# Performance work log

Measured on AMD Instinct MI355X. Metric: run time of the kernel, lower is better.

## Reference

```python
import jax, jax.numpy as jnp
import numpy as np

B, N, D = 512, 22, 3
H, TD, AD, L = 128, 32, 32, 4
SIGMA_DATA = 0.168
NORM_CONST = 1.0
E_IN = 2 * H + 1 + 2  # [h_i, h_j, radial, dist_sq, bond_mask]
NUM_ATOM_TYPES = 4
BONDS = [(0, 1), (1, 2), (1, 3), (1, 4), (4, 5), (4, 6), (6, 7), (6, 8), (8, 9), (8, 10),
         (10, 11), (10, 12), (10, 13), (8, 14), (14, 15), (14, 16), (16, 17), (16, 18),
         (18, 19), (18, 20), (18, 21)]
ATOM_TYPES = [0, 1, 0, 0, 1, 2, 3, 0, 1, 0, 1, 0, 0, 0, 1, 2, 3, 0, 1, 0, 0, 0]


def setup_inputs() -> dict:
    key = jax.random.key(0)
    ks = jax.random.split(key, 16)
    xt = jax.random.normal(ks[0], (B, N, D), jnp.float32)
    xt = xt - xt.mean(axis=1, keepdims=True)  # zero center of mass, per assert_mean_zero
    # EDM-style noise levels, strictly positive (log-normal as in compute_loss)
    t = jnp.exp(jax.random.normal(ks[1], (B,), jnp.float32) * 1.2 - 1.2)
    # fully connected edges without self-loops, batched with node offset b*N
    ii, jj = np.meshgrid(np.arange(N), np.arange(N), indexing='ij')
    msk = ii != jj
    ri, ci = ii[msk], jj[msk]  # (N*(N-1),)
    off = (np.arange(B) * N)[:, None]
    row = jnp.asarray((ri[None] + off).reshape(-1), jnp.int32)
    col = jnp.asarray((ci[None] + off).reshape(-1), jnp.int32)
    adj = np.zeros((N, N), np.float32)
    for a, b in BONDS:
        adj[a, b] = 1.0
        adj[b, a] = 1.0
    bond_mask = jnp.asarray(np.tile(adj[ri, ci], B)[:, None], jnp.float32)  # (E,1)
    atom_types = jnp.asarray(ATOM_TYPES, jnp.int32)

    def lin(k, fi, fo):
        return jax.random.normal(k, (fi, fo), jnp.float32) / np.sqrt(fi)

    def per_layer(k, fi, fo):
        return jax.random.normal(k, (L, fi, fo), jnp.float32) / np.sqrt(fi)

    z = lambda *s: jnp.zeros(s, jnp.float32)
    return dict(
        xt=xt, t=t,
        atom_table=jax.random.normal(ks[2], (NUM_ATOM_TYPES, AD), jnp.float32),
        bond_mask=bond_mask,
        W_in=lin(ks[3], TD + AD, H), b_in=z(H),
        ew1=per_layer(ks[4], E_IN, H), eb1=z(L, H),
        ew2=per_layer(ks[5], H, H), eb2=z(L, H),
        aw=per_layer(ks[6], H, 1), ab=z(L, 1),
        cw1=per_layer(ks[7], H, H), cb1=z(L, H),
        cw2=per_layer(ks[8], H, 1) * 0.1,  # coord head, no bias (xavier-small init)
        nw1=per_layer(ks[9], 2 * H, H), nb1=z(L, H),
        nw2=per_layer(ks[10], H, H), nb2=z(L, H),
        row=row, col=col, atom_types=atom_types,
    )


def _sinusoidal(u, dim):
    half = dim // 2
    freqs = jnp.exp(-jnp.log(10000.0) * jnp.arange(half, dtype=jnp.float32) / half)
    a = u[:, None] * freqs
    return jnp.concatenate([jnp.sin(a), jnp.cos(a)], axis=-1)


def reference(xt, t, atom_table, bond_mask, W_in, b_in, ew1, eb1, ew2, eb2,
              aw, ab, cw1, cb1, cw2, nw1, nb1, nw2, nb2, row, col, atom_types):
    BN = B * N
    act = jax.nn.silu
    # EDM preconditioning
    c_in = 1.0 / jnp.sqrt(t ** 2 + SIGMA_DATA ** 2)
    x = (xt * c_in[:, None, None]).reshape(BN, D)
    # node features: time embedding (broadcast per node) + atom-type embedding
    time_emb = jnp.repeat(_sinusoidal(jnp.log(t) / 4.0, TD), N, axis=0)  # (BN,TD)
    atom_emb = jnp.tile(atom_table[atom_types], (B, 1))                  # (BN,AD)
    h = jnp.concatenate([time_emb, atom_emb], axis=1) @ W_in + b_in      # (BN,H)
    # fixed edge attributes: squared distance at input scale + bond mask
    dist_sq0 = jnp.sum((x[row] - x[col]) ** 2, axis=1, keepdims=True)
    edge_attr = jnp.concatenate([dist_sq0, bond_mask], axis=1)           # (E,2)
    for l in range(L):
        diff = x[row] - x[col]                                           # (E,D)
        radial = jnp.sum(diff ** 2, axis=1, keepdims=True)               # (E,1)
        coord_diff = diff / (jnp.sqrt(radial) + NORM_CONST)
        m = jnp.concatenate([h[row], h[col], radial, edge_attr], axis=1)
        m = act(act(m @ ew1[l] + eb1[l]) @ ew2[l] + eb2[l])              # edge MLP (E,H)
        m = m * jax.nn.sigmoid(m @ aw[l] + ab[l])                        # attention gate
        trans = coord_diff * (act(m @ cw1[l] + cb1[l]) @ cw2[l])         # (E,D)
        x = x + jax.ops.segment_sum(trans, row, num_segments=BN)         # agg='sum'
        agg = jax.ops.segment_sum(m, row, num_segments=BN)               # (BN,H)
        h = h + (act(jnp.concatenate([h, agg], axis=1) @ nw1[l] + nb1[l]) @ nw2[l] + nb2[l])
    x_pred = x.reshape(B, N, D)
    x_pred = x_pred - x_pred.mean(axis=1, keepdims=True)                 # remove_mean
    c_skip = SIGMA_DATA ** 2 / (t ** 2 + SIGMA_DATA ** 2)
    c_out = t * SIGMA_DATA / jnp.sqrt(SIGMA_DATA ** 2 + t ** 2)
    return xt * c_skip[:, None, None] + x_pred * c_out[:, None, None]
```

## Files before the change

kernel.cpp:

```cpp
#include <hip/hip_runtime.h>
#include <math.h>

#define NB 512
#define NNODE 22
#define HH 128
#define NEDGE 462
#define NLAYER 4
#define CHUNK2 128
#define NSUP 4
#define SIG 0.168f

#define ASTR 136
#define NSTR 264
#define BSTR 72
#define SLW (128*72)
#define LSLICES 14
#define STAGE_BYTES 36864
#define NT 1024

typedef __attribute__((ext_vector_type(8))) short short8;
typedef __attribute__((ext_vector_type(4))) short short4v;
typedef __attribute__((ext_vector_type(4))) float f32x4;

#define MFMA_BF16 __builtin_amdgcn_mfma_f32_16x16x32_bf16

__device__ __forceinline__ float siluf(float v) { return v / (1.0f + __expf(-v)); }

__device__ __forceinline__ unsigned short f2bf(float x) {
  union { float f; unsigned u; } v; v.f = x;
  unsigned r = v.u + 0x7FFFu + ((v.u >> 16) & 1u);
  return (unsigned short)(r >> 16);
}
__device__ __forceinline__ float bf2f(unsigned short h) {
  union { unsigned u; float f; } v; v.u = ((unsigned)h) << 16; return v.f;
}
__device__ __forceinline__ void splitbf(float x, unsigned short& hi, unsigned short& lo) {
  union { float f; unsigned u; } v; v.f = x;
  hi = (unsigned short)(v.u >> 16);
  union { unsigned u; float f; } hv; hv.u = ((unsigned)hi) << 16;
  union { float f; unsigned u; } w; w.f = x - hv.f;
  lo = (unsigned short)(w.u >> 16);
}

__global__ void prep_weights(const float* __restrict__ ew1, const float* __restrict__ ew2,
                             const float* __restrict__ cw1, const float* __restrict__ nw1,
                             const float* __restrict__ nw2, unsigned short* __restrict__ ws)
{
  int idx = blockIdx.x * 256 + threadIdx.x;
  if (idx >= 4 * LSLICES * 128 * 72) return;
  int kk = idx % 72; int rest = idx / 72;
  int n = rest % 128; rest /= 128;
  int sl = rest % LSLICES; int l = rest / LSLICES;
  float val = 0.f;
  if (kk < 64) {
    if (sl < 4)       val = ew1[((size_t)l * 259 + sl * 64 + kk) * HH + n];
    else if (sl < 6)  val = ew2[((size_t)l * 128 + (sl - 4) * 64 + kk) * HH + n];
    else if (sl < 8)  val = cw1[((size_t)l * 128 + (sl - 6) * 64 + kk) * HH + n];
    else if (sl < 12) val = nw1[((size_t)l * 256 + (sl - 8) * 64 + kk) * HH + n];
    else              val = nw2[((size_t)l * 128 + (sl - 12) * 64 + kk) * HH + n];
  }
  unsigned short hi, lo;
  { union { float f; unsigned u; } v; v.f = val;
    hi = (unsigned short)(v.u >> 16);
    union { unsigned u; float f; } hv; hv.u = ((unsigned)hi) << 16;
    lo = f2bf(val - hv.f); }
  size_t base = ((size_t)(l * LSLICES + sl) * 2) * SLW + n * BSTR + kk;
  ws[base]       = hi;
  ws[base + SLW] = lo;
}

__global__ __launch_bounds__(NT, 1)
void scorenet_kernel(
    const float* __restrict__ xt, const float* __restrict__ tt,
    const float* __restrict__ atom_table, const float* __restrict__ bond_mask,
    const float* __restrict__ W_in, const float* __restrict__ b_in,
    const float* __restrict__ ew1, const float* __restrict__ eb1,
    const float* __restrict__ eb2,
    const float* __restrict__ aw,  const float* __restrict__ ab,
    const float* __restrict__ cb1, const float* __restrict__ cw2,
    const float* __restrict__ nb1, const float* __restrict__ nb2,
    const int* __restrict__ atom_types,
    const unsigned short* __restrict__ ws,
    float* __restrict__ out)
{
  const int g    = blockIdx.x;
  const int tid  = threadIdx.x;
  const int lane = tid & 63;
  const int wv   = tid >> 6;
  const int ml   = lane & 15;
  const int q    = lane >> 4;
  const int mp   = wv >> 2;
  const int nq   = wv & 3;
  const int mtn  = wv & 1;
  const int nt8  = wv >> 1;

  __shared__ __align__(16) unsigned short sh_B[2 * SLW];
  __shared__ __align__(16) unsigned short sh_Ah[CHUNK2 * ASTR];
  __shared__ __align__(16) unsigned short sh_Al[CHUNK2 * ASTR];
  __shared__ float sh_Phi[2][NNODE * HH];
  __shared__ float sh_h[NNODE * HH];
  __shared__ float sh_agg[NNODE * HH];
  __shared__ float sh_tail[8 * HH];
  __shared__ float sh_awl[HH], sh_cw2l[HH];
  __shared__ float sh_x[NNODE][3], sh_xacc[NNODE][3], sh_x0[NNODE][3];
  __shared__ unsigned char sh_ei[NEDGE];
  __shared__ unsigned char sh_ej[NEDGE];
  __shared__ float sh_cd[3][CHUNK2];
  __shared__ float sh_red[CHUNK2][4];
  __shared__ float sh_gate[CHUNK2];
  __shared__ float sh_tf[32], sh_scal[2], sh_mean[3];

  auto issueB = [&](const unsigned short* src) {
    const char* s8 = (const char*)src;
    char* dbase = (char*)&sh_B[0];
    for (int base = wv * 1024; base < STAGE_BYTES; base += 16384) {
      __builtin_amdgcn_global_load_lds(
          (const __attribute__((address_space(1))) unsigned int*)(s8 + base + lane * 16),
          (__attribute__((address_space(3))) unsigned int*)(dbase + base),
          16, 0, 0);
    }
  };

  auto gemmE = [&](f32x4 (&acc)[2][2], int koff) {
    int arow0 = (mp * 32 + ml) * ASTR + koff;
    int arow1 = arow0 + 16 * ASTR;
#pragma unroll
    for (int sb = 0; sb < 2; sb++) {
      int k8 = sb * 32 + q * 8;
      short8 ah0 = *(const short8*)&sh_Ah[arow0 + k8];
      short8 al0 = *(const short8*)&sh_Al[arow0 + k8];
      short8 ah1 = *(const short8*)&sh_Ah[arow1 + k8];
      short8 al1 = *(const short8*)&sh_Al[arow1 + k8];
#pragma unroll
      for (int t = 0; t < 2; t++) {
        int bi = ((nq * 2 + t) * 16 + ml) * BSTR + k8;
        short8 bh = *(const short8*)&sh_B[bi];
        short8 bl = *(const short8*)&sh_B[SLW + bi];
        acc[0][t] = MFMA_BF16(ah0, bh, acc[0][t], 0, 0, 0);
        acc[0][t] = MFMA_BF16(ah0, bl, acc[0][t], 0, 0, 0);
        acc[0][t] = MFMA_BF16(al0, bh, acc[0][t], 0, 0, 0);
        acc[1][t] = MFMA_BF16(ah1, bh, acc[1][t], 0, 0, 0);
        acc[1][t] = MFMA_BF16(ah1, bl, acc[1][t], 0, 0, 0);
        acc[1][t] = MFMA_BF16(al1, bh, acc[1][t], 0, 0, 0);
      }
    }
  };

  auto gemmN = [&](f32x4& acc, int astr, int koff) {
#pragma unroll
    for (int sb = 0; sb < 2; sb++) {
      int ak = (mtn * 16 + ml) * astr + koff + sb * 32 + q * 8;
      short8 ah = *(const short8*)&sh_Ah[ak];
      short8 al = *(const short8*)&sh_Al[ak];
      int bi = (nt8 * 16 + ml) * BSTR + sb * 32 + q * 8;
      short8 bh = *(const short8*)&sh_B[bi];
      short8 bl = *(const short8*)&sh_B[SLW + bi];
      acc = MFMA_BF16(ah, bh, acc, 0, 0, 0);
      acc = MFMA_BF16(ah, bl, acc, 0, 0, 0);
      acc = MFMA_BF16(al, bh, acc, 0, 0, 0);
    }
  };

  if (tid == 0) {
    float tg = tt[g];
    sh_scal[0] = rsqrtf(tg * tg + SIG * SIG);
    sh_scal[1] = tg;
  }
  __syncthreads();
  const float c_in = sh_scal[0];
  for (int idx = tid; idx < NNODE * 3; idx += NT) {
    float xv = xt[(size_t)g * NNODE * 3 + idx] * c_in;
    sh_x[idx / 3][idx % 3] = xv;
    sh_x0[idx / 3][idx % 3] = xv;
    sh_xacc[idx / 3][idx % 3] = 0.f;
  }
  if (tid < 32) {
    float u = __logf(sh_scal[1]) * 0.25f;
    int   qq = tid & 15;
    float f = __expf((float)qq * -0.5756462732485115f);
    float a = u * f;
    sh_tf[tid] = (tid < 16) ? __sinf(a) : __cosf(a);
  }
  for (int idx = tid; idx < CHUNK2 * ASTR / 2; idx += NT) {
    ((unsigned*)sh_Ah)[idx] = 0u; ((unsigned*)sh_Al)[idx] = 0u;
  }
  for (int e = tid; e < NEDGE; e += NT) {
    int i = e / 21; int r = e - i * 21; int jn = r + (r >= i);
    float bm = bond_mask[(size_t)g * NEDGE + e];
    sh_ei[e] = (unsigned char)(i | ((bm != 0.f) ? 0x80 : 0));
    sh_ej[e] = (unsigned char)jn;
  }
  __syncthreads();
  for (int o = tid; o < HH; o += NT) {
    float s = b_in[o];
#pragma unroll 8
    for (int k = 0; k < 32; k++) s += sh_tf[k] * W_in[k * HH + o];
    sh_agg[o] = s;
  }
  for (int idx = tid; idx < 4 * HH; idx += NT) {
    int a = idx >> 7, o = idx & 127;
    float s = 0.f;
#pragma unroll 8
    for (int k = 0; k < 32; k++) s += atom_table[a * 32 + k] * W_in[(32 + k) * HH + o];
    sh_agg[(1 + a) * HH + o] = s;
  }
  __syncthreads();
  for (int idx = tid; idx < NNODE * HH; idx += NT) {
    int n = idx >> 7, o = idx & 127;
    int at = atom_types[n];
    sh_h[idx] = sh_agg[o] + sh_agg[(1 + at) * HH + o];
  }
  issueB(ws);
  __syncthreads();
  for (int idx = tid; idx < NNODE * HH; idx += NT) sh_agg[idx] = 0.f;

  const f32x4 zf = {0.f, 0.f, 0.f, 0.f};

  for (int l = 0; l < NLAYER; l++) {
    const unsigned short* wsL = ws + (size_t)l * LSLICES * 2 * SLW;
    const float abl = ab[l];

    for (int idx = tid; idx < 8 * HH; idx += NT) {
      int rsel = idx >> 7, n = idx & 127;
      float v;
      switch (rsel) {
        case 0: v = ew1[((size_t)l * 259 + 256) * HH + n]; break;
        case 1: v = ew1[((size_t)l * 259 + 257) * HH + n]; break;
        case 2: v = ew1[((size_t)l * 259 + 258) * HH + n]; break;
        case 3: v = eb1[l * HH + n]; break;
        case 4: v = eb2[l * HH + n]; break;
        case 5: v = cb1[l * HH + n]; break;
        case 6: v = nb1[l * HH + n]; break;
        default: v = nb2[l * HH + n]; break;
      }
      sh_tail[idx] = v;
    }
    if (tid < HH) sh_awl[tid] = aw[l * HH + tid];
    else if (tid < 2 * HH) sh_cw2l[tid - HH] = cw2[l * HH + (tid - HH)];
    for (int idx = tid; idx < NNODE * 16; idx += NT) {
      int nd = idx >> 4, nb = (idx & 15) * 8;
      const float* hp = &sh_h[nd * HH + nb];
      union { short8 v; unsigned short s[8]; } oh, ol;
#pragma unroll
      for (int jj = 0; jj < 8; jj++) { unsigned short hi, lo; splitbf(hp[jj], hi, lo); oh.s[jj] = hi; ol.s[jj] = lo; }
      *(short8*)&sh_Ah[nd * ASTR + nb] = oh.v;
      *(short8*)&sh_Al[nd * ASTR + nb] = ol.v;
    }
    __syncthreads();

    for (int side = 0; side < 2; side++) {
      f32x4 accP = zf;
      for (int s2 = 0; s2 < 2; s2++) {
        gemmN(accP, ASTR, s2 * 64);
        __syncthreads();
        int st = side * 2 + s2;
        issueB(wsL + (st < 3 ? (st + 1) : 4) * 2 * SLW);
        if (s2 == 0) __syncthreads();
      }
      {
        int col = nt8 * 16 + ml;
#pragma unroll
        for (int r = 0; r < 4; r++) {
          int row = mtn * 16 + q * 4 + r;
          if (row < NNODE) sh_Phi[side][row * HH + col] = accP[r];
        }
      }
      __syncthreads();
    }

    for (int sc = 0; sc < NSUP; sc++) {
      const int e0 = sc * CHUNK2;
      {
        int nb = (tid & 15) * 8, eb_ = tid >> 4;
        for (int j4 = 0; j4 < 2; j4++) {
          int el = eb_ + 64 * j4; int e = e0 + el;
          union { short8 v; unsigned short s[8]; } oh, ol;
          if (e < NEDGE) {
            int c = sh_ei[e]; int i = c & 31; int jn = sh_ej[e];
            float bnd = (float)(c >> 7);
            float dx = sh_x[i][0] - sh_x[jn][0];
            float dy = sh_x[i][1] - sh_x[jn][1];
            float dz = sh_x[i][2] - sh_x[jn][2];
            float rad = dx * dx + dy * dy + dz * dz;
            float ex = sh_x0[i][0] - sh_x0[jn][0];
            float ey = sh_x0[i][1] - sh_x0[jn][1];
            float ez = sh_x0[i][2] - sh_x0[jn][2];
            float d0v = ex * ex + ey * ey + ez * ez;
            const float* pi = &sh_Phi[0][i * HH + nb];
            const float* pj = &sh_Phi[1][jn * HH + nb];
#pragma unroll
            for (int jj = 0; jj < 8; jj++) {
              float v = pi[jj] + pj[jj] +
                        rad * sh_tail[nb + jj] + d0v * sh_tail[128 + nb + jj] +
                        bnd * sh_tail[256 + nb + jj] + sh_tail[384 + nb + jj];
              unsigned short hi, lo; splitbf(siluf(v), hi, lo);
              oh.s[jj] = hi; ol.s[jj] = lo;
            }
          } else {
#pragma unroll
            for (int jj = 0; jj < 8; jj++) { oh.s[jj] = 0; ol.s[jj] = 0; }
          }
          *(short8*)&sh_Ah[el * ASTR + nb] = oh.v;
          *(short8*)&sh_Al[el * ASTR + nb] = ol.v;
        }
      }
      __syncthreads();
      f32x4 acc2[2][2];
#pragma unroll
      for (int m2i = 0; m2i < 2; m2i++)
#pragma unroll
        for (int t = 0; t < 2; t++) acc2[m2i][t] = zf;
      gemmE(acc2, 0);
      __syncthreads();
      issueB(wsL + 5 * 2 * SLW);
      if (tid < CHUNK2) {
        int e = e0 + tid;
        if (e < NEDGE) {
          int i = sh_ei[e] & 31, jn = sh_ej[e];
          float dx = sh_x[i][0] - sh_x[jn][0];
          float dy = sh_x[i][1] - sh_x[jn][1];
          float dz = sh_x[i][2] - sh_x[jn][2];
          float inv = 1.0f / (sqrtf(dx * dx + dy * dy + dz * dz) + 1.0f);
          sh_cd[0][tid] = dx * inv; sh_cd[1][tid] = dy * inv; sh_cd[2][tid] = dz * inv;
        } else {
          sh_cd[0][tid] = 0.f; sh_cd[1][tid] = 0.f; sh_cd[2][tid] = 0.f;
        }
      }
      __syncthreads();
      gemmE(acc2, 64);
      __syncthreads();
      issueB(wsL + 6 * 2 * SLW);
      {
        float gpr[2][4];
#pragma unroll
        for (int m2i = 0; m2i < 2; m2i++)
#pragma unroll
          for (int r = 0; r < 4; r++) gpr[m2i][r] = 0.f;
#pragma unroll
        for (int m2i = 0; m2i < 2; m2i++) {
#pragma unroll
          for (int t = 0; t < 2; t++) {
            int col = nq * 32 + t * 16 + ml;
            float eb2c = sh_tail[512 + col], awc = sh_awl[col];
#pragma unroll
            for (int r = 0; r < 4; r++) {
              float v = siluf(acc2[m2i][t][r] + eb2c);
              gpr[m2i][r] += v * awc;
              unsigned short hi, lo; splitbf(v, hi, lo);
              int ai = (mp * 32 + m2i * 16 + q * 4 + r) * ASTR + col;
              sh_Ah[ai] = hi; sh_Al[ai] = lo;
            }
          }
        }
#pragma unroll
        for (int m = 1; m < 16; m <<= 1)
#pragma unroll
          for (int m2i = 0; m2i < 2; m2i++)
#pragma unroll
            for (int r = 0; r < 4; r++) gpr[m2i][r] += __shfl_xor(gpr[m2i][r], m, 64);
        if (ml == 0) {
#pragma unroll
          for (int m2i = 0; m2i < 2; m2i++)
#pragma unroll
            for (int r = 0; r < 4; r++)
              sh_red[mp * 32 + m2i * 16 + q * 4 + r][nq] = gpr[m2i][r];
        }
      }
      __syncthreads();
      if (tid < CHUNK2)
        sh_gate[tid] = 1.0f / (1.0f + __expf(-(sh_red[tid][0] + sh_red[tid][1] +
                                               sh_red[tid][2] + sh_red[tid][3] + abl)));
      f32x4 acc3[2][2];
#pragma unroll
      for (int m2i = 0; m2i < 2; m2i++)
#pragma unroll
        for (int t = 0; t < 2; t++) acc3[m2i][t] = zf;
      gemmE(acc3, 0);
      __syncthreads();
      issueB(wsL + 7 * 2 * SLW);
      int elast = ((e0 + CHUNK2 < NEDGE) ? e0 + CHUNK2 : NEDGE) - 1;
      int i_lo = e0 / 21, i_hi = elast / 21;
      int nrows = i_hi - i_lo + 1;
      for (int idx = tid; idx < nrows * 32; idx += NT) {
        int i = i_lo + (idx >> 5), fb = (idx & 31) * 4;
        int es = i * 21; if (es < e0) es = e0;
        int ee = i * 21 + 21;
        if (ee > e0 + CHUNK2) ee = e0 + CHUNK2;
        if (ee > NEDGE) ee = NEDGE;
        float* ap = &sh_agg[i * HH + fb];
        float a4[4];
#pragma unroll
        for (int c = 0; c < 4; c++) a4[c] = ap[c];
        for (int e = es; e < ee; e++) {
          float gg = sh_gate[e - e0];
          union { short4v v; unsigned short s[4]; } uh, ul;
          uh.v = *(const short4v*)&sh_Ah[(e - e0) * ASTR + fb];
          ul.v = *(const short4v*)&sh_Al[(e - e0) * ASTR + fb];
#pragma unroll
          for (int c = 0; c < 4; c++) a4[c] += gg * (bf2f(uh.s[c]) + bf2f(ul.s[c]));
        }
#pragma unroll
        for (int c = 0; c < 4; c++) ap[c] = a4[c];
      }
      __syncthreads();
      gemmE(acc3, 64);
      __syncthreads();
      issueB(sc < 3 ? wsL + 4 * 2 * SLW : wsL + 8 * 2 * SLW);
      {
        float cs[2][4];
#pragma unroll
        for (int m2i = 0; m2i < 2; m2i++) {
          float g4[4];
#pragma unroll
          for (int r = 0; r < 4; r++) {
            g4[r] = sh_gate[mp * 32 + m2i * 16 + q * 4 + r];
            cs[m2i][r] = 0.f;
          }
#pragma unroll
          for (int t = 0; t < 2; t++) {
            int col = nq * 32 + t * 16 + ml;
            float cb1c = sh_tail[640 + col], cwc = sh_cw2l[col];
#pragma unroll
            for (int r = 0; r < 4; r++)
              cs[m2i][r] += siluf(g4[r] * acc3[m2i][t][r] + cb1c) * cwc;
          }
        }
#pragma unroll
        for (int m = 1; m < 16; m <<= 1)
#pragma unroll
          for (int m2i = 0; m2i < 2; m2i++)
#pragma unroll
            for (int r = 0; r < 4; r++) cs[m2i][r] += __shfl_xor(cs[m2i][r], m, 64);
        if (ml == 0) {
#pragma unroll
          for (int m2i = 0; m2i < 2; m2i++)
#pragma unroll
            for (int r = 0; r < 4; r++)
              sh_red[mp * 32 + m2i * 16 + q * 4 + r][nq] = cs[m2i][r];
        }
      }
      __syncthreads();
      for (int idx = tid; idx < nrows * 3; idx += NT) {
        int i = i_lo + idx / 3, d = idx % 3;
        int es = i * 21; if (es < e0) es = e0;
        int ee = i * 21 + 21;
        if (ee > e0 + CHUNK2) ee = e0 + CHUNK2;
        if (ee > NEDGE) ee = NEDGE;
        float s = 0.f;
        for (int e = es; e < ee; e++) {
          const float* rd = sh_red[e - e0];
          s += sh_cd[d][e - e0] * (rd[0] + rd[1] + rd[2] + rd[3]);
        }
        sh_xacc[i][d] += s;
      }
    }

    for (int idx = tid; idx < NNODE * 32; idx += NT) {
      int nd = idx >> 5, kb = (idx & 31) * 8;
      const float* src = (kb < 128) ? &sh_h[nd * HH + kb] : &sh_agg[nd * HH + (kb - 128)];
      union { short8 v; unsigned short s[8]; } oh, ol;
#pragma unroll
      for (int jj = 0; jj < 8; jj++) { unsigned short hi, lo; splitbf(src[jj], hi, lo); oh.s[jj] = hi; ol.s[jj] = lo; }
      *(short8*)&sh_Ah[nd * NSTR + kb] = oh.v;
      *(short8*)&sh_Al[nd * NSTR + kb] = ol.v;
    }
    __syncthreads();
    {
      f32x4 n1a = zf;
      for (int s = 0; s < 4; s++) {
        gemmN(n1a, NSTR, s * 64);
        __syncthreads();
        issueB(wsL + (s < 3 ? (9 + s) : 12) * 2 * SLW);
        if (s < 3) __syncthreads();
      }
      {
        int col = nt8 * 16 + ml;
        float nb1c = sh_tail[768 + col];
#pragma unroll
        for (int r = 0; r < 4; r++) {
          int row = mtn * 16 + q * 4 + r;
          if (row < NNODE) {
            unsigned short hi, lo; splitbf(siluf(n1a[r] + nb1c), hi, lo);
            sh_Ah[row * ASTR + col] = hi; sh_Al[row * ASTR + col] = lo;
          }
        }
      }
      __syncthreads();
      f32x4 n2a = zf;
      gemmN(n2a, ASTR, 0);
      __syncthreads();
      issueB(wsL + 13 * 2 * SLW);
      for (int idx = tid; idx < NNODE * 3; idx += NT) {
        int n = idx / 3, d = idx % 3;
        sh_x[n][d] += sh_xacc[n][d];
        sh_xacc[n][d] = 0.f;
      }
      for (int idx = tid; idx < NNODE * HH; idx += NT) sh_agg[idx] = 0.f;
      __syncthreads();
      gemmN(n2a, ASTR, 64);
      __syncthreads();
      if (l < 3) issueB(ws + (size_t)(l + 1) * LSLICES * 2 * SLW);
      {
        int col = nt8 * 16 + ml;
        float nb2c = sh_tail[896 + col];
#pragma unroll
        for (int r = 0; r < 4; r++) {
          int row = mtn * 16 + q * 4 + r;
          if (row < NNODE) sh_h[row * HH + col] += n2a[r] + nb2c;
        }
      }
    }
    __syncthreads();
  }

  if (tid < 3) {
    float s = 0.f;
    for (int n = 0; n < NNODE; n++) s += sh_x[n][tid];
    sh_mean[tid] = s * (1.0f / NNODE);
  }
  __syncthreads();
  {
    float tg = sh_scal[1];
    float den = tg * tg + SIG * SIG;
    float c_skip = (SIG * SIG) / den;
    float c_out  = tg * SIG * rsqrtf(den);
    for (int idx = tid; idx < NNODE * 3; idx += NT) {
      int n = idx / 3, d = idx % 3;
      out[(size_t)g * NNODE * 3 + idx] =
          xt[(size_t)g * NNODE * 3 + idx] * c_skip + (sh_x[n][d] - sh_mean[d]) * c_out;
    }
  }
}

extern "C" void kernel_launch(void* const* d_in, const int* in_sizes, int n_in,
                              void* d_out, int out_size, void* d_ws, size_t ws_size,
                              hipStream_t stream) {
  const float* xt         = (const float*)d_in[0];
  const float* t          = (const float*)d_in[1];
  const float* atom_table = (const float*)d_in[2];
  const float* bond_mask  = (const float*)d_in[3];
  const float* W_in       = (const float*)d_in[4];
  const float* b_in       = (const float*)d_in[5];
  const float* ew1        = (const float*)d_in[6];
  const float* eb1        = (const float*)d_in[7];
  const float* ew2        = (const float*)d_in[8];
  const float* eb2        = (const float*)d_in[9];
  const float* aw         = (const float*)d_in[10];
  const float* ab         = (const float*)d_in[11];
  const float* cw1        = (const float*)d_in[12];
  const float* cb1        = (const float*)d_in[13];
  const float* cw2        = (const float*)d_in[14];
  const float* nw1        = (const float*)d_in[15];
  const float* nb1        = (const float*)d_in[16];
  const float* nw2        = (const float*)d_in[17];
  const float* nb2        = (const float*)d_in[18];
  const int* atom_types   = (const int*)d_in[21];

  unsigned short* ws = (unsigned short*)d_ws;

  prep_weights<<<2016, 256, 0, stream>>>(ew1, ew2, cw1, nw1, nw2, ws);

  scorenet_kernel<<<NB, NT, 0, stream>>>(
      xt, t, atom_table, bond_mask, W_in, b_in,
      ew1, eb1, eb2, aw, ab, cb1, cw2, nb1, nb2,
      atom_types, ws, (float*)d_out);
}
```

Before: 751.7 us.

## Shrink edge chunk to 96 and block to 768 threads for multi-block occupancy

Cuts the edge chunk from 128 to 96 edges (5 super-chunks instead of 4) and the block from 16 to 12 waves, with launch bounds asking for 3 blocks per CU. The node GEMMs are remapped so that 4 waves each compute two output tiles, keeping full coverage with fewer waves. The aim is to fit several blocks per CU so that one block's barriers and load waits can overlap with another's compute. In exchange there are more chunk iterations and barriers per layer, and the register limit implied by the new launch bounds may cause spills. Whether the shared-memory footprint actually allows 3 resident blocks is unclear.

```diff
diff --git a/kernel.cpp b/kernel.cpp
--- a/kernel.cpp
+++ b/kernel.cpp
@@ -6,8 +6,8 @@
 #define HH 128
 #define NEDGE 462
 #define NLAYER 4
-#define CHUNK2 128
-#define NSUP 4
+#define EC 96
+#define NSUP 5
 #define SIG 0.168f
 
 #define ASTR 136
@@ -16,7 +16,7 @@
 #define SLW (128*72)
 #define LSLICES 14
 #define STAGE_BYTES 36864
-#define NT 1024
+#define NT 768
 
 typedef __attribute__((ext_vector_type(8))) short short8;
 typedef __attribute__((ext_vector_type(4))) short short4v;
@@ -69,7 +69,7 @@
   ws[base + SLW] = lo;
 }
 
-__global__ __launch_bounds__(NT, 1)
+__global__ __launch_bounds__(NT, 3)
 void scorenet_kernel(
     const float* __restrict__ xt, const float* __restrict__ tt,
     const float* __restrict__ atom_table, const float* __restrict__ bond_mask,
@@ -91,12 +91,14 @@
   const int q    = lane >> 4;
   const int mp   = wv >> 2;
   const int nq   = wv & 3;
-  const int mtn  = wv & 1;
-  const int nt8  = wv >> 1;
+  const int m0t  = wv >> 3;
+  const int n0t  = wv & 7;
+  const bool dual = (wv < 4);
+  const int n1t  = wv + 4;
 
   __shared__ __align__(16) unsigned short sh_B[2 * SLW];
-  __shared__ __align__(16) unsigned short sh_Ah[CHUNK2 * ASTR];
-  __shared__ __align__(16) unsigned short sh_Al[CHUNK2 * ASTR];
+  __shared__ __align__(16) unsigned short sh_Ah[EC * ASTR];
+  __shared__ __align__(16) unsigned short sh_Al[EC * ASTR];
   __shared__ float sh_Phi[2][NNODE * HH];
   __shared__ float sh_h[NNODE * HH];
   __shared__ float sh_agg[NNODE * HH];
@@ -105,15 +107,15 @@
   __shared__ float sh_x[NNODE][3], sh_xacc[NNODE][3], sh_x0[NNODE][3];
   __shared__ unsigned char sh_ei[NEDGE];
   __shared__ unsigned char sh_ej[NEDGE];
-  __shared__ float sh_cd[3][CHUNK2];
-  __shared__ float sh_red[CHUNK2][4];
-  __shared__ float sh_gate[CHUNK2];
+  __shared__ float sh_cd[3][EC];
+  __shared__ float sh_red[EC][4];
+  __shared__ float sh_gate[EC];
   __shared__ float sh_tf[32], sh_scal[2], sh_mean[3];
 
   auto issueB = [&](const unsigned short* src) {
     const char* s8 = (const char*)src;
     char* dbase = (char*)&sh_B[0];
-    for (int base = wv * 1024; base < STAGE_BYTES; base += 16384) {
+    for (int base = wv * 1024; base < STAGE_BYTES; base += 12288) {
       __builtin_amdgcn_global_load_lds(
           (const __attribute__((address_space(1))) unsigned int*)(s8 + base + lane * 16),
           (__attribute__((address_space(3))) unsigned int*)(dbase + base),
@@ -146,18 +148,28 @@
     }
   };
 
-  auto gemmN = [&](f32x4& acc, int astr, int koff) {
+  auto gemmN = [&](f32x4& acc0, f32x4& acc1, int astr, int koff) {
 #pragma unroll
     for (int sb = 0; sb < 2; sb++) {
-      int ak = (mtn * 16 + ml) * astr + koff + sb * 32 + q * 8;
-      short8 ah = *(const short8*)&sh_Ah[ak];
-      short8 al = *(const short8*)&sh_Al[ak];
-      int bi = (nt8 * 16 + ml) * BSTR + sb * 32 + q * 8;
-      short8 bh = *(const short8*)&sh_B[bi];
-      short8 bl = *(const short8*)&sh_B[SLW + bi];
-      acc = MFMA_BF16(ah, bh, acc, 0, 0, 0);
-      acc = MFMA_BF16(ah, bl, acc, 0, 0, 0);
-      acc = MFMA_BF16(al, bh, acc, 0, 0, 0);
+      int k8 = koff + sb * 32 + q * 8;
+      short8 ah0 = *(const short8*)&sh_Ah[(m0t * 16 + ml) * astr + k8];
+      short8 al0 = *(const short8*)&sh_Al[(m0t * 16 + ml) * astr + k8];
+      int bi0 = (n0t * 16 + ml) * BSTR + sb * 32 + q * 8;
+      short8 bh0 = *(const short8*)&sh_B[bi0];
+      short8 bl0 = *(const short8*)&sh_B[SLW + bi0];
+      acc0 = MFMA_BF16(ah0, bh0, acc0, 0, 0, 0);
+      acc0 = MFMA_BF16(ah0, bl0, acc0, 0, 0, 0);
+      acc0 = MFMA_BF16(al0, bh0, acc0, 0, 0, 0);
+      if (dual) {
+        short8 ah1 = *(const short8*)&sh_Ah[(16 + ml) * astr + k8];
+        short8 al1 = *(const short8*)&sh_Al[(16 + ml) * astr + k8];
+        int bi1 = (n1t * 16 + ml) * BSTR + sb * 32 + q * 8;
+        short8 bh1 = *(const short8*)&sh_B[bi1];
+        short8 bl1 = *(const short8*)&sh_B[SLW + bi1];
+        acc1 = MFMA_BF16(ah1, bh1, acc1, 0, 0, 0);
+        acc1 = MFMA_BF16(ah1, bl1, acc1, 0, 0, 0);
+        acc1 = MFMA_BF16(al1, bh1, acc1, 0, 0, 0);
+      }
     }
   };
 
@@ -181,7 +193,7 @@
     float a = u * f;
     sh_tf[tid] = (tid < 16) ? __sinf(a) : __cosf(a);
   }
-  for (int idx = tid; idx < CHUNK2 * ASTR / 2; idx += NT) {
+  for (int idx = tid; idx < EC * ASTR / 2; idx += NT) {
     ((unsigned*)sh_Ah)[idx] = 0u; ((unsigned*)sh_Al)[idx] = 0u;
   }
   for (int e = tid; e < NEDGE; e += NT) {
@@ -249,31 +261,39 @@
     __syncthreads();
 
     for (int side = 0; side < 2; side++) {
-      f32x4 accP = zf;
+      f32x4 accP0 = zf, accP1 = zf;
       for (int s2 = 0; s2 < 2; s2++) {
-        gemmN(accP, ASTR, s2 * 64);
+        gemmN(accP0, accP1, ASTR, s2 * 64);
         __syncthreads();
         int st = side * 2 + s2;
         issueB(wsL + (st < 3 ? (st + 1) : 4) * 2 * SLW);
         if (s2 == 0) __syncthreads();
       }
       {
-        int col = nt8 * 16 + ml;
+        int col = n0t * 16 + ml;
 #pragma unroll
         for (int r = 0; r < 4; r++) {
-          int row = mtn * 16 + q * 4 + r;
-          if (row < NNODE) sh_Phi[side][row * HH + col] = accP[r];
+          int row = m0t * 16 + q * 4 + r;
+          if (row < NNODE) sh_Phi[side][row * HH + col] = accP0[r];
+        }
+        if (dual) {
+          int col1 = n1t * 16 + ml;
+#pragma unroll
+          for (int r = 0; r < 4; r++) {
+            int row = 16 + q * 4 + r;
+            if (row < NNODE) sh_Phi[side][row * HH + col1] = accP1[r];
+          }
         }
       }
       __syncthreads();
     }
 
     for (int sc = 0; sc < NSUP; sc++) {
-      const int e0 = sc * CHUNK2;
+      const int e0 = sc * EC;
       {
         int nb = (tid & 15) * 8, eb_ = tid >> 4;
         for (int j4 = 0; j4 < 2; j4++) {
-          int el = eb_ + 64 * j4; int e = e0 + el;
+          int el = eb_ + 48 * j4; int e = e0 + el;
           union { short8 v; unsigned short s[8]; } oh, ol;
           if (e < NEDGE) {
             int c = sh_ei[e]; int i = c & 31; int jn = sh_ej[e];
@@ -313,7 +333,7 @@
       gemmE(acc2, 0);
       __syncthreads();
       issueB(wsL + 5 * 2 * SLW);
-      if (tid < CHUNK2) {
+      if (tid < EC) {
         int e = e0 + tid;
         if (e < NEDGE) {
           int i = sh_ei[e] & 31, jn = sh_ej[e];
@@ -367,7 +387,7 @@
         }
       }
       __syncthreads();
-      if (tid < CHUNK2)
+      if (tid < EC)
         sh_gate[tid] = 1.0f / (1.0f + __expf(-(sh_red[tid][0] + sh_red[tid][1] +
                                                sh_red[tid][2] + sh_red[tid][3] + abl)));
       f32x4 acc3[2][2];
@@ -378,14 +398,14 @@
       gemmE(acc3, 0);
       __syncthreads();
       issueB(wsL + 7 * 2 * SLW);
-      int elast = ((e0 + CHUNK2 < NEDGE) ? e0 + CHUNK2 : NEDGE) - 1;
+      int elast = ((e0 + EC < NEDGE) ? e0 + EC : NEDGE) - 1;
       int i_lo = e0 / 21, i_hi = elast / 21;
       int nrows = i_hi - i_lo + 1;
       for (int idx = tid; idx < nrows * 32; idx += NT) {
         int i = i_lo + (idx >> 5), fb = (idx & 31) * 4;
         int es = i * 21; if (es < e0) es = e0;
         int ee = i * 21 + 21;
-        if (ee > e0 + CHUNK2) ee = e0 + CHUNK2;
+        if (ee > e0 + EC) ee = e0 + EC;
         if (ee > NEDGE) ee = NEDGE;
         float* ap = &sh_agg[i * HH + fb];
         float a4[4];
@@ -405,7 +425,7 @@
       __syncthreads();
       gemmE(acc3, 64);
       __syncthreads();
-      issueB(sc < 3 ? wsL + 4 * 2 * SLW : wsL + 8 * 2 * SLW);
+      issueB(sc < NSUP - 1 ? wsL + 4 * 2 * SLW : wsL + 8 * 2 * SLW);
       {
         float cs[2][4];
 #pragma unroll
@@ -444,7 +464,7 @@
         int i = i_lo + idx / 3, d = idx % 3;
         int es = i * 21; if (es < e0) es = e0;
         int ee = i * 21 + 21;
-        if (ee > e0 + CHUNK2) ee = e0 + CHUNK2;
+        if (ee > e0 + EC) ee = e0 + EC;
         if (ee > NEDGE) ee = NEDGE;
         float s = 0.f;
         for (int e = es; e < ee; e++) {
@@ -466,28 +486,40 @@
     }
     __syncthreads();
     {
-      f32x4 n1a = zf;
+      f32x4 n1a0 = zf, n1a1 = zf;
       for (int s = 0; s < 4; s++) {
-        gemmN(n1a, NSTR, s * 64);
+        gemmN(n1a0, n1a1, NSTR, s * 64);
         __syncthreads();
         issueB(wsL + (s < 3 ? (9 + s) : 12) * 2 * SLW);
         if (s < 3) __syncthreads();
       }
       {
-        int col = nt8 * 16 + ml;
+        int col = n0t * 16 + ml;
         float nb1c = sh_tail[768 + col];
 #pragma unroll
         for (int r = 0; r < 4; r++) {
-          int row = mtn * 16 + q * 4 + r;
+          int row = m0t * 16 + q * 4 + r;
           if (row < NNODE) {
-            unsigned short hi, lo; splitbf(siluf(n1a[r] + nb1c), hi, lo);
+            unsigned short hi, lo; splitbf(siluf(n1a0[r] + nb1c), hi, lo);
             sh_Ah[row * ASTR + col] = hi; sh_Al[row * ASTR + col] = lo;
           }
         }
-      }
-      __syncthreads();
-      f32x4 n2a = zf;
-      gemmN(n2a, ASTR, 0);
+        if (dual) {
+          int col1 = n1t * 16 + ml;
+          float nb1c1 = sh_tail[768 + col1];
+#pragma unroll
+          for (int r = 0; r < 4; r++) {
+            int row = 16 + q * 4 + r;
+            if (row < NNODE) {
+              unsigned short hi, lo; splitbf(siluf(n1a1[r] + nb1c1), hi, lo);
+              sh_Ah[row * ASTR + col1] = hi; sh_Al[row * ASTR + col1] = lo;
+            }
+          }
+        }
+      }
+      __syncthreads();
+      f32x4 n2a0 = zf, n2a1 = zf;
+      gemmN(n2a0, n2a1, ASTR, 0);
       __syncthreads();
       issueB(wsL + 13 * 2 * SLW);
       for (int idx = tid; idx < NNODE * 3; idx += NT) {
@@ -497,16 +529,25 @@
       }
       for (int idx = tid; idx < NNODE * HH; idx += NT) sh_agg[idx] = 0.f;
       __syncthreads();
-      gemmN(n2a, ASTR, 64);
+      gemmN(n2a0, n2a1, ASTR, 64);
       __syncthreads();
       if (l < 3) issueB(ws + (size_t)(l + 1) * LSLICES * 2 * SLW);
       {
-        int col = nt8 * 16 + ml;
+        int col = n0t * 16 + ml;
         float nb2c = sh_tail[896 + col];
 #pragma unroll
         for (int r = 0; r < 4; r++) {
-          int row = mtn * 16 + q * 4 + r;
-          if (row < NNODE) sh_h[row * HH + col] += n2a[r] + nb2c;
+          int row = m0t * 16 + q * 4 + r;
+          if (row < NNODE) sh_h[row * HH + col] += n2a0[r] + nb2c;
+        }
+        if (dual) {
+          int col1 = n1t * 16 + ml;
+          float nb2c1 = sh_tail[896 + col1];
+#pragma unroll
+          for (int r = 0; r < 4; r++) {
+            int row = 16 + q * 4 + r;
+            if (row < NNODE) sh_h[row * HH + col1] += n2a1[r] + nb2c1;
+          }
         }
       }
     }
```

Result: slower. 768.5 us (+2.2%).
